# Performance work log

Measured on AMD Instinct MI355X. Metric: run time of the kernel, lower is better.

## Reference

```python
import jax, jax.numpy as jnp
import numpy as np

B, T, H, L = 64, 1024, 256, 1


def setup_inputs() -> dict:
    key = jax.random.key(0)
    ks = jax.random.split(key, 20)
    s = 1.0 / np.sqrt(H)

    def u(k, shape):
        return jax.random.uniform(k, shape, jnp.float32, -s, s)

    return {
        "inputs": jax.random.normal(ks[0], (B, T, H), jnp.float32),
        "hidden_states": jax.random.normal(ks[1], (L, B, H), jnp.float32),
        # Attn params: W is Linear(2H -> H), V is Linear(H -> H)
        "W_w": u(ks[2], (H, 2 * H)), "W_b": u(ks[3], (H,)),
        "V_w": u(ks[4], (H, H)), "V_b": u(ks[5], (H,)),
        # GRU params (input_size == hidden_size)
        "w_ir": u(ks[6], (H, H)), "w_iz": u(ks[7], (H, H)), "w_in": u(ks[8], (H, H)),
        "b_ir": u(ks[9], (H,)), "b_iz": u(ks[10], (H,)), "b_in": u(ks[11], (H,)),
        "w_hr": u(ks[12], (H, H)), "w_hz": u(ks[13], (H, H)), "w_hn": u(ks[14], (H, H)),
        "b_hr": u(ks[15], (H,)), "b_hz": u(ks[16], (H,)), "b_hn": u(ks[17], (H,)),
    }


def reference(inputs, hidden_states, W_w, W_b, V_w, V_b,
              w_ir, w_iz, w_in, b_ir, b_iz, b_in,
              w_hr, w_hz, w_hn, b_hr, b_hz, b_hn):
    h = inputs.shape[-1]
    # ---- Attn: score_t = sum_l V(tanh(W([h_l ; x_t]))) ----
    # Split W over the concat: first H cols act on hidden, last H on input.
    W_hid, W_inp = W_w[:, :h], W_w[:, h:]
    hp = jnp.einsum('lbh,kh->lbk', hidden_states, W_hid)      # (L,B,H)
    xp = jnp.einsum('bth,kh->tbk', inputs, W_inp)             # (T,B,H)
    z = jnp.tanh(hp[:, None] + xp[None] + W_b)                # (L,T,B,H)
    scores = jnp.einsum('ltbh,kh->tbk', z, V_w) + inputs.shape[0] * 0.0  # (T,B,H) pre-bias
    scores = scores + V_b * hidden_states.shape[0]            # V bias summed over L layers
    scores = jnp.swapaxes(scores, 0, 1)                       # (B,T,H)
    sm = jax.nn.softmax(scores, axis=1)                       # softmax over seq dim
    ctx = scores * sm                                         # (B,T,H) attention-weighted features
    x_attn = sm.sum(axis=2)                                   # (B,T)

    # ---- GRU over ctx (faithful: outputs[0]=h0, recurrence starts at t=1) ----
    h0 = hidden_states[0]                                     # (B,H)
    xr = jnp.einsum('bth,kh->tbk', ctx, w_ir) + b_ir          # (T,B,H)
    xz = jnp.einsum('bth,kh->tbk', ctx, w_iz) + b_iz
    xn = jnp.einsum('bth,kh->tbk', ctx, w_in) + b_in

    def step(h_prev, xs):
        xr_t, xz_t, xn_t = xs
        r = jax.nn.sigmoid(xr_t + h_prev @ w_hr.T + b_hr)
        n = jnp.tanh(xn_t + r * (h_prev @ w_hn.T + b_hn))
        zt = jax.nn.sigmoid(xz_t + h_prev @ w_hz.T + b_hz)
        h_new = (1.0 - zt) * n + zt * h_prev
        return h_new, h_new

    h_last, hs = jax.lax.scan(step, h0, (xr[1:], xz[1:], xn[1:]))
    outs = jnp.concatenate([h0[None], hs], axis=0)            # (T,B,H)
    outputs = jnp.swapaxes(outs, 0, 1)                        # (B,T,H)
    return outputs, h_last[None], x_attn
```

## Files before the change

### kernel.cpp

```cpp
#include <hip/hip_runtime.h>

#define DEVI __device__ __forceinline__

typedef float  f32x4  __attribute__((ext_vector_type(4)));
typedef __bf16 bf16x8 __attribute__((ext_vector_type(8)));
typedef unsigned short u16x8 __attribute__((ext_vector_type(8)));

DEVI unsigned short f2bf(float f) {
    unsigned u = __builtin_bit_cast(unsigned, f);
    unsigned r = (u + 0x7fffu + ((u >> 16) & 1u)) >> 16;
    return (unsigned short)r;
}
DEVI float bf2f(unsigned short s) {
    return __builtin_bit_cast(float, (unsigned)s << 16);
}
DEVI u16x8 pack8(float4 a, float4 b) {
    u16x8 p;
    p[0] = f2bf(a.x); p[1] = f2bf(a.y); p[2] = f2bf(a.z); p[3] = f2bf(a.w);
    p[4] = f2bf(b.x); p[5] = f2bf(b.y); p[6] = f2bf(b.z); p[7] = f2bf(b.w);
    return p;
}
DEVI f32x4 mfma16(u16x8 a, u16x8 b, f32x4 c) {
    return __builtin_amdgcn_mfma_f32_16x16x32_bf16(
        __builtin_bit_cast(bf16x8, a), __builtin_bit_cast(bf16x8, b), c, 0, 0, 0);
}
DEVI float sigm(float x)   { return 1.f / (1.f + __expf(-x)); }
DEVI float tanh_f(float x) { return 1.f - 2.f / (1.f + __expf(2.f * x)); }

#define Hh 256
#define Bb 64
#define Tt 1024
#define MROWS (Bb * Tt)

__global__ __launch_bounds__(256) void hp_kernel(const float* __restrict__ hid,
                                                 const float* __restrict__ Ww,
                                                 float* __restrict__ hp) {
    int b = blockIdx.x, k = threadIdx.x;
    __shared__ __align__(16) float hs[Hh];
    hs[k] = hid[b * Hh + k];
    __syncthreads();
    const float4* w4 = (const float4*)(Ww + (size_t)k * 512);
    const float4* h4 = (const float4*)hs;
    float acc = 0.f;
#pragma unroll 8
    for (int i = 0; i < 64; i++) {
        float4 a = w4[i], x = h4[i];
        acc += a.x * x.x + a.y * x.y + a.z * x.z + a.w * x.w;
    }
    hp[b * Hh + k] = acc;
}

__global__ __launch_bounds__(256) void bias_prep(const float* __restrict__ b_ir,
                                                 const float* __restrict__ b_hr,
                                                 const float* __restrict__ b_iz,
                                                 const float* __restrict__ b_hz,
                                                 float* __restrict__ cb) {
    int k = threadIdx.x;
    cb[k] = b_ir[k] + b_hr[k];
    cb[256 + k] = b_iz[k] + b_hz[k];
}

template <int EPI, bool ABF16>
__global__ __launch_bounds__(512) void gemm_k(
    const void* __restrict__ Aab,
    const float* __restrict__ W0, const float* __restrict__ W1, const float* __restrict__ W2,
    int wstride, int wcoloff,
    const float* __restrict__ bv0, const float* __restrict__ bv1, const float* __restrict__ bv2,
    const float* __restrict__ hp, const float* __restrict__ Wb,
    void* __restrict__ outv) {
    __shared__ __align__(16) unsigned short As[128 * 256];
    __shared__ __align__(16) unsigned short Bs[64 * 256];

    int tid = threadIdx.x;
    int bx = blockIdx.x, by = blockIdx.y;
    int mat = (EPI == 2) ? (by >> 2) : 0;
    int cb  = (EPI == 2) ? (by & 3) : by;
    int rowBase = bx * 128, colBase = cb * 64;
    const float* W  = (mat == 0) ? W0 : ((mat == 1) ? W1 : W2);
    const float* bv = (mat == 0) ? bv0 : ((mat == 1) ? bv1 : bv2);

    if (ABF16) {
        const unsigned short* A = (const unsigned short*)Aab;
#pragma unroll
        for (int i = 0; i < 8; i++) {
            int idx = i * 512 + tid, r = idx >> 5, g = idx & 31, gs = g ^ (r & 7);
            *(uint4*)&As[r * 256 + gs * 8] =
                *(const uint4*)(A + (((size_t)(rowBase + r)) << 8) + g * 8);
        }
    } else {
        const float* A = (const float*)Aab;
#pragma unroll
        for (int i = 0; i < 8; i++) {
            int idx = i * 512 + tid, r = idx >> 5, g = idx & 31, gs = g ^ (r & 7);
            const float* s = A + (((size_t)(rowBase + r)) << 8) + g * 8;
            float4 f0 = *(const float4*)s, f1 = *(const float4*)(s + 4);
            *(u16x8*)&As[r * 256 + gs * 8] = pack8(f0, f1);
        }
    }
#pragma unroll
    for (int i = 0; i < 4; i++) {
        int idx = i * 512 + tid, r = idx >> 5, g = idx & 31, gs = g ^ (r & 7);
        const float* s = W + (size_t)(colBase + r) * wstride + wcoloff + g * 8;
        float4 f0 = *(const float4*)s, f1 = *(const float4*)(s + 4);
        *(u16x8*)&Bs[r * 256 + gs * 8] = pack8(f0, f1);
    }
    __syncthreads();

    int wid = tid >> 6, lane = tid & 63, l15 = lane & 15, grp = lane >> 4;
    int wr = (wid >> 1) * 32, wc = (wid & 1) * 32;
    f32x4 acc[2][2] = {};
#pragma unroll
    for (int kc = 0; kc < 8; kc++) {
        u16x8 a[2], bb[2];
#pragma unroll
        for (int rt = 0; rt < 2; rt++) {
            int r = wr + rt * 16 + l15;
            int gs = (kc * 4 + grp) ^ (r & 7);
            a[rt] = *(const u16x8*)&As[r * 256 + gs * 8];
        }
#pragma unroll
        for (int ct = 0; ct < 2; ct++) {
            int r = wc + ct * 16 + l15;
            int gs = (kc * 4 + grp) ^ (r & 7);
            bb[ct] = *(const u16x8*)&Bs[r * 256 + gs * 8];
        }
#pragma unroll
        for (int rt = 0; rt < 2; rt++)
#pragma unroll
            for (int ct = 0; ct < 2; ct++)
                acc[rt][ct] = mfma16(a[rt], bb[ct], acc[rt][ct]);
    }
#pragma unroll
    for (int rt = 0; rt < 2; rt++)
#pragma unroll
        for (int ct = 0; ct < 2; ct++)
#pragma unroll
            for (int i = 0; i < 4; i++) {
                int rl = wr + rt * 16 + grp * 4 + i;
                int cl = wc + ct * 16 + l15;
                size_t r = (size_t)rowBase + rl;
                int c = colBase + cl;
                float v = acc[rt][ct][i];
                if (EPI == 0) {
                    v = tanh_f(v + hp[(r >> 10) * 256 + c] + Wb[c]);
                    ((unsigned short*)outv)[r * 256 + c] = f2bf(v);
                } else if (EPI == 1) {
                    ((float*)outv)[r * 256 + c] = v + bv[c];
                } else {
                    size_t t = r & 1023, b = r >> 10;
                    ((unsigned short*)outv)[(size_t)mat * 16777216 + (t * 64 + b) * 256 + c] =
                        f2bf(v + bv[c]);
                }
            }
}

__global__ __launch_bounds__(256) void softmax_pass1(const float* __restrict__ scores,
                                                     float* __restrict__ partMS) {
    int b = blockIdx.x, tc = blockIdx.y, k = threadIdx.x;
    const float* p = scores + ((size_t)b * Tt + tc * 128) * Hh + k;
    float m = -1e30f, S = 0.f;
    for (int i = 0; i < 128; i++) {
        float s = p[(size_t)i * Hh];
        float mn = fmaxf(m, s);
        S = S * __expf(m - mn) + __expf(s - mn);
        m = mn;
    }
    int idx = (b * 8 + tc) * Hh + k;
    partMS[idx * 2] = m;
    partMS[idx * 2 + 1] = S;
}

__global__ __launch_bounds__(256) void softmax_pass2(const float* __restrict__ scores,
                                                     const float* __restrict__ partMS,
                                                     unsigned short* __restrict__ ctx,
                                                     float* __restrict__ x_attn) {
    int b = blockIdx.x, tc = blockIdx.y;
    int tid = threadIdx.x, w = tid >> 6, lane = tid & 63;
    float mj[4], Sj[4];
#pragma unroll
    for (int j = 0; j < 4; j++) {
        int k = lane + j * 64;
        float m = -1e30f;
#pragma unroll
        for (int c = 0; c < 8; c++)
            m = fmaxf(m, partMS[((b * 8 + c) * Hh + k) * 2]);
        float S = 0.f;
#pragma unroll
        for (int c = 0; c < 8; c++) {
            int idx = (b * 8 + c) * Hh + k;
            S += partMS[idx * 2 + 1] * __expf(partMS[idx * 2] - m);
        }
        mj[j] = m;
        Sj[j] = 1.f / S;
    }
    for (int i = 0; i < 32; i++) {
        int t = tc * 128 + w * 32 + i;
        const float* sp = scores + ((size_t)b * Tt + t) * Hh;
        unsigned short* cp = ctx + ((size_t)b * Tt + t) * Hh;
        float accsm = 0.f;
#pragma unroll
        for (int j = 0; j < 4; j++) {
            int k = lane + j * 64;
            float s = sp[k];
            float sm = __expf(s - mj[j]) * Sj[j];
            accsm += sm;
            cp[k] = f2bf(s * sm);
        }
#pragma unroll
        for (int o = 32; o >= 1; o >>= 1) accsm += __shfl_xor(accsm, o, 64);
        if (lane == 0) x_attn[b * Tt + t] = accsm;
    }
}

__global__ __attribute__((amdgpu_flat_work_group_size(512, 512),
                          amdgpu_waves_per_eu(2, 2)))
void scan_gru(
    const unsigned short* __restrict__ xg,
    const float* __restrict__ whr, const float* __restrict__ whz, const float* __restrict__ whn,
    const float* __restrict__ bhn,
    const float* __restrict__ hidden,
    float* __restrict__ outputs, float* __restrict__ hlast) {
    __shared__ __align__(16) unsigned short wn_lds[65536];
    __shared__ __align__(16) unsigned short hb[2][Hh];
    int b = blockIdx.x;
    int tid = threadIdx.x, w = tid >> 6, lane = tid & 63;
    int l15 = lane & 15, grp = lane >> 4;

    for (int it = 0; it < 16; ++it) {
        int q = it * 512 + tid;
        int col = q >> 5, c = q & 31;
        const float* s = whn + (size_t)col * Hh + c * 8;
        float4 f0 = *(const float4*)s, f1 = *(const float4*)(s + 4);
        *(u16x8*)&wn_lds[col * 256 + ((c ^ (col & 7)) * 8)] = pack8(f0, f1);
    }

    u16x8 wfr[2][8], wfz[2][8];
#pragma unroll
    for (int ct = 0; ct < 2; ct++) {
        int col = w * 32 + ct * 16 + l15;
#pragma unroll
        for (int kc = 0; kc < 8; kc++) {
            const float* s1 = whr + (size_t)col * Hh + kc * 32 + grp * 8;
            wfr[ct][kc] = pack8(*(const float4*)s1, *(const float4*)(s1 + 4));
            const float* s2 = whz + (size_t)col * Hh + kc * 32 + grp * 8;
            wfz[ct][kc] = pack8(*(const float4*)s2, *(const float4*)(s2 + 4));
        }
    }
    asm volatile("" : "+a"(wfr[0][0]), "+a"(wfr[0][1]), "+a"(wfr[0][2]), "+a"(wfr[0][3]),
                      "+a"(wfr[0][4]), "+a"(wfr[0][5]), "+a"(wfr[0][6]), "+a"(wfr[0][7]));
    asm volatile("" : "+a"(wfr[1][0]), "+a"(wfr[1][1]), "+a"(wfr[1][2]), "+a"(wfr[1][3]),
                      "+a"(wfr[1][4]), "+a"(wfr[1][5]), "+a"(wfr[1][6]), "+a"(wfr[1][7]));
    asm volatile("" : "+a"(wfz[0][0]), "+a"(wfz[0][1]), "+a"(wfz[0][2]), "+a"(wfz[0][3]),
                      "+a"(wfz[0][4]), "+a"(wfz[0][5]), "+a"(wfz[0][6]), "+a"(wfz[0][7]));
    asm volatile("" : "+a"(wfz[1][0]), "+a"(wfz[1][1]), "+a"(wfz[1][2]), "+a"(wfz[1][3]),
                      "+a"(wfz[1][4]), "+a"(wfz[1][5]), "+a"(wfz[1][6]), "+a"(wfz[1][7]));

    int col0 = w * 32 + l15, col1 = col0 + 16;
    int nb0 = col0 * 256, nx0s = col0 & 7;
    int nb1 = col1 * 256, nx1s = col1 & 7;
    float bhn0 = 0.f, bhn1 = 0.f, hp0 = 0.f, hp1 = 0.f;
    if (lane < 16) {
        bhn0 = bhn[col0];
        bhn1 = bhn[col1];
        hp0 = hidden[b * Hh + col0];
        hp1 = hidden[b * Hh + col1];
        hb[0][col0] = f2bf(hp0);
        hb[0][col1] = f2bf(hp1);
        outputs[((size_t)b * Tt) * Hh + col0] = hp0;
        outputs[((size_t)b * Tt) * Hh + col1] = hp1;
    }
    const unsigned short* xr = xg;
    const unsigned short* xz = xg + 16777216;
    const unsigned short* xn = xg + 33554432;
    unsigned short px0 = 0, px1 = 0, px2 = 0, px3 = 0, px4 = 0, px5 = 0;
    if (lane < 16) {
        size_t off = ((size_t)64 + b) * Hh;
        px0 = xr[off + col0]; px1 = xr[off + col1];
        px2 = xz[off + col0]; px3 = xz[off + col1];
        px4 = xn[off + col0]; px5 = xn[off + col1];
    }
    __syncthreads();

    int p = 0;
    for (int t = 1; t < Tt; t++) {
        unsigned short cx0 = px0, cx1 = px1, cx2 = px2, cx3 = px3, cx4 = px4, cx5 = px5;
        int tnext = (t + 1 < Tt) ? t + 1 : t;
        if (lane < 16) {
            size_t off = ((size_t)tnext * 64 + b) * Hh;
            px0 = xr[off + col0]; px1 = xr[off + col1];
            px2 = xz[off + col0]; px3 = xz[off + col1];
            px4 = xn[off + col0]; px5 = xn[off + col1];
        }
        f32x4 ar0 = {0.f, 0.f, 0.f, 0.f}, ar1 = {0.f, 0.f, 0.f, 0.f};
        f32x4 az0 = {0.f, 0.f, 0.f, 0.f}, az1 = {0.f, 0.f, 0.f, 0.f};
        f32x4 an0 = {0.f, 0.f, 0.f, 0.f}, an1 = {0.f, 0.f, 0.f, 0.f};
#pragma unroll
        for (int kc = 0; kc < 8; kc++) {
            u16x8 af = *(const u16x8*)&hb[p][kc * 32 + grp * 8];
            ar0 = mfma16(af, wfr[0][kc], ar0);
            ar1 = mfma16(af, wfr[1][kc], ar1);
            az0 = mfma16(af, wfz[0][kc], az0);
            az1 = mfma16(af, wfz[1][kc], az1);
            int c = kc * 4 + grp;
            u16x8 wn0 = *(const u16x8*)&wn_lds[nb0 + ((c ^ nx0s) * 8)];
            u16x8 wn1 = *(const u16x8*)&wn_lds[nb1 + ((c ^ nx1s) * 8)];
            an0 = mfma16(af, wn0, an0);
            an1 = mfma16(af, wn1, an1);
        }
        if (lane < 16) {
            float r0 = sigm(bf2f(cx0) + ar0[0]);
            float r1 = sigm(bf2f(cx1) + ar1[0]);
            float z0 = sigm(bf2f(cx2) + az0[0]);
            float z1 = sigm(bf2f(cx3) + az1[0]);
            float n0 = tanh_f(bf2f(cx4) + r0 * (an0[0] + bhn0));
            float n1 = tanh_f(bf2f(cx5) + r1 * (an1[0] + bhn1));
            float hn0 = (1.f - z0) * n0 + z0 * hp0;
            float hn1 = (1.f - z1) * n1 + z1 * hp1;
            hb[p ^ 1][col0] = f2bf(hn0);
            hb[p ^ 1][col1] = f2bf(hn1);
            size_t ro = ((size_t)b * Tt + t) * Hh;
            outputs[ro + col0] = hn0;
            outputs[ro + col1] = hn1;
            hp0 = hn0;
            hp1 = hn1;
        }
        p ^= 1;
        asm volatile("s_waitcnt lgkmcnt(0)" ::: "memory");
        __builtin_amdgcn_s_barrier();
        asm volatile("" ::: "memory");
    }
    if (lane < 16) {
        hlast[b * Hh + col0] = hp0;
        hlast[b * Hh + col1] = hp1;
    }
}

extern "C" void kernel_launch(void* const* d_in, const int* in_sizes, int n_in,
                              void* d_out, int out_size, void* d_ws, size_t ws_size,
                              hipStream_t stream) {
    const float* inputs = (const float*)d_in[0];
    const float* hidden = (const float*)d_in[1];
    const float* W_w  = (const float*)d_in[2];
    const float* W_b  = (const float*)d_in[3];
    const float* V_w  = (const float*)d_in[4];
    const float* V_b  = (const float*)d_in[5];
    const float* w_ir = (const float*)d_in[6];
    const float* w_iz = (const float*)d_in[7];
    const float* w_in = (const float*)d_in[8];
    const float* b_ir = (const float*)d_in[9];
    const float* b_iz = (const float*)d_in[10];
    const float* b_in = (const float*)d_in[11];
    const float* w_hr = (const float*)d_in[12];
    const float* w_hz = (const float*)d_in[13];
    const float* w_hn = (const float*)d_in[14];
    const float* b_hr = (const float*)d_in[15];
    const float* b_hz = (const float*)d_in[16];
    const float* b_hn = (const float*)d_in[17];

    float* hp = (float*)d_ws;
    float* partMS = hp + 65536;
    float* cbias = partMS + 262144;
    unsigned short* zbuf = (unsigned short*)(cbias + 512);
    unsigned short* ctx = zbuf;
    unsigned short* xgb = zbuf + 16777216;

    float* scores  = (float*)d_out;
    float* outputs = (float*)d_out;
    float* hlast   = outputs + 16777216;
    float* x_attn  = hlast + 16384;

    hp_kernel<<<64, 256, 0, stream>>>(hidden, W_w, hp);
    bias_prep<<<1, 256, 0, stream>>>(b_ir, b_hr, b_iz, b_hz, cbias);

    gemm_k<0, false><<<dim3(512, 4), 512, 0, stream>>>(
        inputs, W_w, nullptr, nullptr, 512, 256,
        nullptr, nullptr, nullptr, hp, W_b, zbuf);

    gemm_k<1, true><<<dim3(512, 4), 512, 0, stream>>>(
        zbuf, V_w, nullptr, nullptr, 256, 0,
        V_b, nullptr, nullptr, nullptr, nullptr, scores);

    softmax_pass1<<<dim3(64, 8), 256, 0, stream>>>(scores, partMS);
    softmax_pass2<<<dim3(64, 8), 256, 0, stream>>>(scores, partMS, ctx, x_attn);

    gemm_k<2, true><<<dim3(512, 12), 512, 0, stream>>>(
        ctx, w_ir, w_iz, w_in, 256, 0,
        cbias, cbias + 256, b_in, nullptr, nullptr, xgb);

    scan_gru<<<64, 512, 0, stream>>>(
        xgb, w_hr, w_hz, w_hn, b_hn, hidden, outputs, hlast);
}
```

Baseline: 1.637 ms.

## Store W_hn in LDS fragment-major order and spread GRU gate math over 32 lanes

```diff
diff --git a/kernel.cpp b/kernel.cpp
--- a/kernel.cpp
+++ b/kernel.cpp
@@ -224,20 +224,21 @@
     __shared__ __align__(16) unsigned short hb[2][Hh];
     int b = blockIdx.x;
     int tid = threadIdx.x, w = tid >> 6, lane = tid & 63;
-    int l15 = lane & 15, grp = lane >> 4;
+    int grp = lane >> 4;
 
     for (int it = 0; it < 16; ++it) {
         int q = it * 512 + tid;
-        int col = q >> 5, c = q & 31;
-        const float* s = whn + (size_t)col * Hh + c * 8;
-        float4 f0 = *(const float4*)s, f1 = *(const float4*)(s + 4);
-        *(u16x8*)&wn_lds[col * 256 + ((c ^ (col & 7)) * 8)] = pack8(f0, f1);
+        int frag = q >> 6, lslot = q & 63;
+        int col = ((frag >> 3) << 4) | (lslot & 15);
+        int koff = (frag & 7) * 32 + (lslot >> 4) * 8;
+        const float* s = whn + (size_t)col * Hh + koff;
+        *(u16x8*)&wn_lds[frag * 512 + lslot * 8] = pack8(*(const float4*)s, *(const float4*)(s + 4));
     }
 
     u16x8 wfr[2][8], wfz[2][8];
 #pragma unroll
     for (int ct = 0; ct < 2; ct++) {
-        int col = w * 32 + ct * 16 + l15;
+        int col = w * 32 + ct * 16 + (lane & 15);
 #pragma unroll
         for (int kc = 0; kc < 8; kc++) {
             const float* s1 = whr + (size_t)col * Hh + kc * 32 + grp * 8;
@@ -255,41 +256,32 @@
     asm volatile("" : "+a"(wfz[1][0]), "+a"(wfz[1][1]), "+a"(wfz[1][2]), "+a"(wfz[1][3]),
                       "+a"(wfz[1][4]), "+a"(wfz[1][5]), "+a"(wfz[1][6]), "+a"(wfz[1][7]));
 
-    int col0 = w * 32 + l15, col1 = col0 + 16;
-    int nb0 = col0 * 256, nx0s = col0 & 7;
-    int nb1 = col1 * 256, nx1s = col1 & 7;
-    float bhn0 = 0.f, bhn1 = 0.f, hp0 = 0.f, hp1 = 0.f;
-    if (lane < 16) {
-        bhn0 = bhn[col0];
-        bhn1 = bhn[col1];
-        hp0 = hidden[b * Hh + col0];
-        hp1 = hidden[b * Hh + col1];
-        hb[0][col0] = f2bf(hp0);
-        hb[0][col1] = f2bf(hp1);
-        outputs[((size_t)b * Tt) * Hh + col0] = hp0;
-        outputs[((size_t)b * Tt) * Hh + col1] = hp1;
+    int mycol = w * 32 + (lane & 31);
+    int wnb = (w * 16) * 512 + lane * 8;
+    float bhnS = 0.f, hpS = 0.f;
+    if (lane < 32) {
+        bhnS = bhn[mycol];
+        hpS = hidden[b * Hh + mycol];
+        hb[0][mycol] = f2bf(hpS);
+        outputs[((size_t)b * Tt) * Hh + mycol] = hpS;
     }
     const unsigned short* xr = xg;
     const unsigned short* xz = xg + 16777216;
     const unsigned short* xn = xg + 33554432;
-    unsigned short px0 = 0, px1 = 0, px2 = 0, px3 = 0, px4 = 0, px5 = 0;
-    if (lane < 16) {
-        size_t off = ((size_t)64 + b) * Hh;
-        px0 = xr[off + col0]; px1 = xr[off + col1];
-        px2 = xz[off + col0]; px3 = xz[off + col1];
-        px4 = xn[off + col0]; px5 = xn[off + col1];
+    unsigned short pxr = 0, pxz = 0, pxn = 0;
+    if (lane < 32) {
+        size_t off = ((size_t)64 + b) * Hh + mycol;
+        pxr = xr[off]; pxz = xz[off]; pxn = xn[off];
     }
     __syncthreads();
 
     int p = 0;
     for (int t = 1; t < Tt; t++) {
-        unsigned short cx0 = px0, cx1 = px1, cx2 = px2, cx3 = px3, cx4 = px4, cx5 = px5;
+        unsigned short cxr = pxr, cxz = pxz, cxn = pxn;
         int tnext = (t + 1 < Tt) ? t + 1 : t;
-        if (lane < 16) {
-            size_t off = ((size_t)tnext * 64 + b) * Hh;
-            px0 = xr[off + col0]; px1 = xr[off + col1];
-            px2 = xz[off + col0]; px3 = xz[off + col1];
-            px4 = xn[off + col0]; px5 = xn[off + col1];
+        if (lane < 32) {
+            size_t off = ((size_t)tnext * 64 + b) * Hh + mycol;
+            pxr = xr[off]; pxz = xz[off]; pxn = xn[off];
         }
         f32x4 ar0 = {0.f, 0.f, 0.f, 0.f}, ar1 = {0.f, 0.f, 0.f, 0.f};
         f32x4 az0 = {0.f, 0.f, 0.f, 0.f}, az1 = {0.f, 0.f, 0.f, 0.f};
@@ -301,37 +293,33 @@
             ar1 = mfma16(af, wfr[1][kc], ar1);
             az0 = mfma16(af, wfz[0][kc], az0);
             az1 = mfma16(af, wfz[1][kc], az1);
-            int c = kc * 4 + grp;
-            u16x8 wn0 = *(const u16x8*)&wn_lds[nb0 + ((c ^ nx0s) * 8)];
-            u16x8 wn1 = *(const u16x8*)&wn_lds[nb1 + ((c ^ nx1s) * 8)];
+            u16x8 wn0 = *(const u16x8*)&wn_lds[wnb + kc * 512];
+            u16x8 wn1 = *(const u16x8*)&wn_lds[wnb + 8 * 512 + kc * 512];
             an0 = mfma16(af, wn0, an0);
             an1 = mfma16(af, wn1, an1);
         }
-        if (lane < 16) {
-            float r0 = sigm(bf2f(cx0) + ar0[0]);
-            float r1 = sigm(bf2f(cx1) + ar1[0]);
-            float z0 = sigm(bf2f(cx2) + az0[0]);
-            float z1 = sigm(bf2f(cx3) + az1[0]);
-            float n0 = tanh_f(bf2f(cx4) + r0 * (an0[0] + bhn0));
-            float n1 = tanh_f(bf2f(cx5) + r1 * (an1[0] + bhn1));
-            float hn0 = (1.f - z0) * n0 + z0 * hp0;
-            float hn1 = (1.f - z1) * n1 + z1 * hp1;
-            hb[p ^ 1][col0] = f2bf(hn0);
-            hb[p ^ 1][col1] = f2bf(hn1);
-            size_t ro = ((size_t)b * Tt + t) * Hh;
-            outputs[ro + col0] = hn0;
-            outputs[ro + col1] = hn1;
-            hp0 = hn0;
-            hp1 = hn1;
+        float vr = __shfl(ar1[0], lane & 15);
+        float vz = __shfl(az1[0], lane & 15);
+        float vn = __shfl(an1[0], lane & 15);
+        float gr = (lane < 16) ? ar0[0] : vr;
+        float gz = (lane < 16) ? az0[0] : vz;
+        float gn = (lane < 16) ? an0[0] : vn;
+        if (lane < 32) {
+            float r0 = sigm(bf2f(cxr) + gr);
+            float z0 = sigm(bf2f(cxz) + gz);
+            float n0 = tanh_f(bf2f(cxn) + r0 * (gn + bhnS));
+            float hn = (1.f - z0) * n0 + z0 * hpS;
+            hb[p ^ 1][mycol] = f2bf(hn);
+            outputs[((size_t)b * Tt + t) * Hh + mycol] = hn;
+            hpS = hn;
         }
         p ^= 1;
         asm volatile("s_waitcnt lgkmcnt(0)" ::: "memory");
         __builtin_amdgcn_s_barrier();
         asm volatile("" ::: "memory");
     }
-    if (lane < 16) {
-        hlast[b * Hh + col0] = hp0;
-        hlast[b * Hh + col1] = hp1;
+    if (lane < 32) {
+        hlast[b * Hh + mycol] = hpS;
     }
 }
 
```

Measured after the change: 1.477 ms. -9.8%, faster.
